# Kernel optimization log

Hardware: AMD Instinct MI355X
Metric: run time of the kernel (lower is better)

Reference implementation:

```python
import jax, jax.numpy as jnp
import numpy as np

EPS = 1e-5
HD = 16          # hidden_dim
OC = 256         # out_chs
NH = 8           # num_heads (groups of qkv conv)
DV = OC // (2 * HD)  # per-head value dim = 8


def conv_bn_silu(x, w, gamma, beta, mean, var, stride=1, pad=1, groups=1):
    # Conv2d(bias=False) + BatchNorm2d(eval) + SiLU, NCHW/OIHW
    y = jax.lax.conv_general_dilated(
        x, w, (stride, stride), [(pad, pad), (pad, pad)],
        dimension_numbers=('NCHW', 'OIHW', 'NCHW'),
        feature_group_count=groups)
    inv = gamma * jax.lax.rsqrt(var + EPS)
    y = y * inv[None, :, None, None] + (beta - mean * inv)[None, :, None, None]
    return y * jax.nn.sigmoid(y)


def _bn_params(key, c):
    k1, k2, k3, k4 = jax.random.split(key, 4)
    g = 1.0 + 0.1 * jax.random.normal(k1, (c,), jnp.float32)
    b = 0.1 * jax.random.normal(k2, (c,), jnp.float32)
    m = 0.1 * jax.random.normal(k3, (c,), jnp.float32)
    v = jax.random.uniform(k4, (c,), jnp.float32, 0.5, 1.5)
    return g, b, m, v


def setup_inputs() -> dict:
    key = jax.random.key(0)
    ks = jax.random.split(key, 8)
    B, C, H, W = 16, 256, 80, 80
    qkv_out = HD * 2 + OC // 2  # 160
    d = {}
    d['x'] = jax.random.normal(ks[0], (B, C, H, W), jnp.float32)
    # qkv_conv: grouped 3x3, groups=NH -> in per group = C//NH
    d['qkv_w'] = jax.random.normal(ks[1], (qkv_out, C // NH, 3, 3), jnp.float32) * 0.05
    d['qkv_g'], d['qkv_b'], d['qkv_m'], d['qkv_v'] = _bn_params(ks[2], qkv_out)
    # hidden_conv: dense 3x3
    d['hid_w'] = jax.random.normal(ks[3], (OC, C, 3, 3), jnp.float32) * 0.02
    d['hid_g'], d['hid_b'], d['hid_m'], d['hid_v'] = _bn_params(ks[4], OC)
    # out_conv: 1x1 on (OC//2*3) channels
    d['out_w'] = jax.random.normal(ks[5], (OC, OC // 2 * 3, 1, 1), jnp.float32) * 0.05
    d['out_g'], d['out_b'], d['out_m'], d['out_v'] = _bn_params(ks[6], OC)
    return d


def reference(x, qkv_w, qkv_g, qkv_b, qkv_m, qkv_v,
              hid_w, hid_g, hid_b, hid_m, hid_v,
              out_w, out_g, out_b, out_m, out_v):
    B, C, H, W = x.shape
    N = H * W
    qkv = conv_bn_silu(x, qkv_w, qkv_g, qkv_b, qkv_m, qkv_v, stride=1, pad=1, groups=NH)
    q = qkv[:, :HD]               # (B, HD, H, W)
    k = qkv[:, HD:2 * HD]
    v = qkv[:, 2 * HD:]           # (B, OC//2, H, W)
    # permute to (B, N, HD) / (B, N, HD, DV), channel-major reshape matches torch .view
    q = q.transpose(0, 2, 3, 1).reshape(B, N, HD)
    k = k.transpose(0, 2, 3, 1).reshape(B, N, HD)
    v = v.transpose(0, 2, 3, 1).reshape(B, N, HD, DV)
    # per-pixel tiny attention: attn[b,n,i,j] = softmax_j(q_i * k_j)
    attn = jax.nn.softmax(q[..., :, None] * k[..., None, :], axis=-1)  # (B,N,HD,HD)
    y = jnp.einsum('bnij,bnjd->bnid', attn, v)                          # (B,N,HD,DV)
    # torch: permute(0,2,3,1).view(B, OC//2, H, W)
    y = y.transpose(0, 2, 3, 1).reshape(B, OC // 2, H, W)
    h = conv_bn_silu(x, hid_w, hid_g, hid_b, hid_m, hid_v, stride=1, pad=1)
    y = jnp.concatenate([y, h], axis=1)  # (B, OC//2*3, H, W)
    return conv_bn_silu(y, out_w, out_g, out_b, out_m, out_v, stride=1, pad=0)
```

## Files before the change

### kernel.cpp

```cpp
#include <hip/hip_runtime.h>
#include <stdint.h>

typedef unsigned short u16;
typedef unsigned int u32;
typedef __attribute__((ext_vector_type(4))) float f32x4;
typedef __attribute__((ext_vector_type(8))) __bf16 bf16x8;

#define EPS_BN 1e-5f

__device__ __forceinline__ u16 f2bf(float f) {
  u32 u = __builtin_bit_cast(u32, f);
  u32 r = (u + 0x7fffu + ((u >> 16) & 1u)) >> 16;
  return (u16)r;
}

__device__ __forceinline__ float silu_f(float v) {
  return v / (1.0f + __expf(-v));
}

__device__ __forceinline__ void gll16(const void* g, void* l) {
  __builtin_amdgcn_global_load_lds(
      (__attribute__((address_space(1))) void*)(void*)g,
      (__attribute__((address_space(3))) void*)l, 16, 0, 0);
}

__global__ __launch_bounds__(256) void prep(
    const float* __restrict__ qkv_w, const float* __restrict__ qg,
    const float* __restrict__ qb, const float* __restrict__ qm,
    const float* __restrict__ qv,
    const float* __restrict__ hid_w, const float* __restrict__ hg,
    const float* __restrict__ hb, const float* __restrict__ hm,
    const float* __restrict__ hv,
    const float* __restrict__ out_w, const float* __restrict__ og,
    const float* __restrict__ ob, const float* __restrict__ om,
    const float* __restrict__ ov,
    u16* __restrict__ wtb, u16* __restrict__ w2b, u16* __restrict__ wqp,
    float* __restrict__ bnq_s, float* __restrict__ bnq_b,
    float* __restrict__ bnh_s, float* __restrict__ bnh_b,
    float* __restrict__ bn2s, float* __restrict__ bn2b,
    float* __restrict__ zpg)
{
  const int gid = blockIdx.x * 256 + threadIdx.x;
  if (gid < 256 * 2304) {
    int j = gid / 2304, k = gid - j * 2304;
    int tap = k >> 8, c = k & 255;
    wtb[gid] = f2bf(hid_w[(j * 256 + c) * 9 + tap]);
  }
  if (gid < 73728) {
    int g = gid / 9216;
    int r = gid - g * 9216;
    int j = r / 288, k = r - j * 288;
    int tap = k >> 5, cg = k & 31;
    float v = 0.f;
    if (j < 20) v = qkv_w[((g * 20 + j) * 32 + cg) * 9 + tap];
    wqp[gid] = f2bf(v);
  }
  if (gid < 98304) w2b[gid] = f2bf(out_w[gid]);
  if (gid < 160) {
    float iv = qg[gid] * rsqrtf(qv[gid] + EPS_BN);
    bnq_s[gid] = iv; bnq_b[gid] = qb[gid] - qm[gid] * iv;
  }
  if (gid < 256) {
    float iv = hg[gid] * rsqrtf(hv[gid] + EPS_BN);
    bnh_s[gid] = iv; bnh_b[gid] = hb[gid] - hm[gid] * iv;
    float iv2 = og[gid] * rsqrtf(ov[gid] + EPS_BN);
    bn2s[gid] = iv2; bn2b[gid] = ob[gid] - om[gid] * iv2;
  }
  if (gid < 64) zpg[gid] = 0.f;
}

__global__ __launch_bounds__(256) void nchw2nhwc(
    const float* __restrict__ x, u16* __restrict__ xn)
{
  __shared__ u16 T[80 * 66];
  const int t = threadIdx.x;
  const int ct = blockIdx.x;
  const int h  = blockIdx.y;
  const int b  = blockIdx.z;
  const float* src = x + ((size_t)b * 256 + ct * 64) * 6400 + h * 80;
  for (int it = 0; it < 5; ++it) {
    int idx = it * 256 + t;
    int cl = idx / 20, w4 = idx - cl * 20;
    float4 v = *(const float4*)(src + (size_t)cl * 6400 + w4 * 4);
    T[(w4 * 4 + 0) * 66 + cl] = f2bf(v.x);
    T[(w4 * 4 + 1) * 66 + cl] = f2bf(v.y);
    T[(w4 * 4 + 2) * 66 + cl] = f2bf(v.z);
    T[(w4 * 4 + 3) * 66 + cl] = f2bf(v.w);
  }
  __syncthreads();
  u16* dst = xn + ((size_t)(b * 80 + h) * 80) * 256 + ct * 64;
  for (int it = 0; it < 5; ++it) {
    int idx = it * 256 + t;
    int wl = idx >> 4;
    int cl = (idx & 15) * 4;
    ushort4 v4;
    v4.x = T[wl * 66 + cl + 0];
    v4.y = T[wl * 66 + cl + 1];
    v4.z = T[wl * 66 + cl + 2];
    v4.w = T[wl * 66 + cl + 3];
    *(ushort4*)(dst + (size_t)wl * 256 + cl) = v4;
  }
}

__global__ __launch_bounds__(256, 2) void gemm_main(
    const u16* __restrict__ xn, const u16* __restrict__ wt,
    const float* __restrict__ bns, const float* __restrict__ bnb,
    const float* __restrict__ zpg, u16* __restrict__ ycat)
{
  __shared__ __attribute__((aligned(16))) u16 Al[128 * 64];
  __shared__ __attribute__((aligned(16))) u16 Bl[128 * 64];
  const int t = threadIdx.x;
  const int wave = t >> 6, lane = t & 63;
  const int wr = wave >> 1, wc = wave & 1;
  const int orig = blockIdx.y * 2 + blockIdx.x;
  const int wg = (orig & 7) * 200 + (orig >> 3);
  const int jtile = (wg / 800) * 128;
  const int ptile = (wg % 800) * 128;

  const int srcc = (((lane & 7) ^ ((lane >> 3) & 7)) * 8);
  int pb[4], hh[4], wwv[4], bofB[4];
#pragma unroll
  for (int c = 0; c < 4; ++c) {
    int m = wave * 32 + c * 8 + (lane >> 3);
    int p = ptile + m;
    pb[c] = p;
    int hw = p % 6400;
    hh[c] = hw / 80;
    wwv[c] = hw - (hw / 80) * 80;
    bofB[c] = (jtile + m) * 2304 + srcc;
  }
  u16* AlW = Al + wave * 2048;
  u16* BlW = Bl + wave * 2048;

  f32x4 acc[4][4];
#pragma unroll
  for (int m = 0; m < 4; ++m)
#pragma unroll
    for (int n = 0; n < 4; ++n) {
      f32x4 z = {0.f, 0.f, 0.f, 0.f};
      acc[m][n] = z;
    }

  for (int ks = 0; ks < 36; ++ks) {
    const int k0 = ks * 64;
    const int tap = k0 >> 8;
    const int c0 = k0 & 255;
    const int dh = tap / 3 - 1, dw = tap - (tap / 3) * 3 - 1;
    __syncthreads();
#pragma unroll
    for (int c = 0; c < 4; ++c) {
      int h2 = hh[c] + dh, w2 = wwv[c] + dw;
      bool ok = ((unsigned)h2 < 80u) & ((unsigned)w2 < 80u);
      const u16* src = ok
          ? (xn + ((size_t)(pb[c] + dh * 80 + dw) * 256 + c0 + srcc))
          : (const u16*)zpg;
      gll16(src, AlW + c * 512);
    }
#pragma unroll
    for (int c = 0; c < 4; ++c)
      gll16(wt + (size_t)(bofB[c] + k0), BlW + c * 512);
    __syncthreads();
#pragma unroll
    for (int kk = 0; kk < 2; ++kk) {
      const int q = kk * 4 + (lane >> 4);
      const int c16 = lane & 15;
      bf16x8 av[4], bv[4];
#pragma unroll
      for (int m = 0; m < 4; ++m) {
        int r = wr * 64 + m * 16 + c16;
        av[m] = *(const bf16x8*)(Al + r * 64 + (q ^ (r & 7)) * 8);
      }
#pragma unroll
      for (int n = 0; n < 4; ++n) {
        int r = wc * 64 + n * 16 + c16;
        bv[n] = *(const bf16x8*)(Bl + r * 64 + (q ^ (r & 7)) * 8);
      }
#pragma unroll
      for (int m = 0; m < 4; ++m)
#pragma unroll
        for (int n = 0; n < 4; ++n)
          acc[m][n] = __builtin_amdgcn_mfma_f32_16x16x32_bf16(
              av[m], bv[n], acc[m][n], 0, 0, 0);
    }
  }

  const int c16 = lane & 15, rg = lane >> 4;
#pragma unroll
  for (int n = 0; n < 4; ++n) {
    int j = jtile + wc * 64 + n * 16 + c16;
    float sc = bns[j], bi = bnb[j];
#pragma unroll
    for (int m = 0; m < 4; ++m) {
      int p0 = ptile + wr * 64 + m * 16 + rg * 4;
#pragma unroll
      for (int r = 0; r < 4; ++r) {
        float v = silu_f(acc[m][n][r] * sc + bi);
        ycat[(size_t)(p0 + r) * 384 + 128 + j] = f2bf(v);
      }
    }
  }
}

__global__ __launch_bounds__(256, 2) void qkv_gemm(
    const u16* __restrict__ xn, const u16* __restrict__ wqp,
    const float* __restrict__ bnq_s, const float* __restrict__ bnq_b,
    const float* __restrict__ zpg, float* __restrict__ qkvb)
{
  __shared__ __attribute__((aligned(16))) u16 Al[2][128 * 64];
  const int t = threadIdx.x;
  const int wave = t >> 6, lane = t & 63;
  const int orig = blockIdx.x;
  const int wg = (orig & 7) * 100 + (orig >> 3);
  const int ptile = wg * 128;

  const int srcc = (((lane & 7) ^ ((lane >> 3) & 7)) * 8);
  int pb[4], hh[4], wwv[4];
#pragma unroll
  for (int c = 0; c < 4; ++c) {
    int m = wave * 32 + c * 8 + (lane >> 3);
    int p = ptile + m;
    pb[c] = p;
    int hw = p % 6400;
    hh[c] = hw / 80;
    wwv[c] = hw - (hw / 80) * 80;
  }
  u16* AlW0 = Al[0] + wave * 2048;
  u16* AlW1 = Al[1] + wave * 2048;

  const int q = lane >> 4, c16 = lane & 15;

  auto STAGE = [&](int tap, int cc, u16* dst) {
    if (tap > 8) tap = 8;
    const int dh = tap / 3 - 1, dw = tap - (tap / 3) * 3 - 1;
    const int dp = dh * 80 + dw;
    const int c0 = cc * 64;
#pragma unroll
    for (int c = 0; c < 4; ++c) {
      int h2 = hh[c] + dh, w2 = wwv[c] + dw;
      bool ok = ((unsigned)h2 < 80u) & ((unsigned)w2 < 80u);
      const u16* src = ok
          ? (xn + ((size_t)(pb[c] + dp) * 256 + c0 + srcc))
          : (const u16*)zpg;
      gll16(src, dst + c * 512);
    }
  };
  auto BQ = [&](int tap, int cc, bf16x8* bv) {
    if (tap > 8) tap = 8;
#pragma unroll
    for (int h = 0; h < 2; ++h)
#pragma unroll
      for (int nf = 0; nf < 2; ++nf) {
        int row = (2 * cc + h) * 32 + nf * 16 + c16;
        bv[h * 2 + nf] =
            *(const bf16x8*)(wqp + (size_t)row * 288 + tap * 32 + q * 8);
      }
  };

  f32x4 acc[2][16];
#pragma unroll
  for (int m = 0; m < 2; ++m)
#pragma unroll
    for (int f = 0; f < 16; ++f) {
      f32x4 z = {0.f, 0.f, 0.f, 0.f};
      acc[m][f] = z;
    }

  bf16x8 bqA[4], bqB[4];
  BQ(0, 0, bqA);
  STAGE(0, 0, AlW0);

  for (int tap = 0; tap < 9; ++tap) {
#pragma unroll
    for (int cc = 0; cc < 4; ++cc) {
      const int ntap = (cc == 3) ? tap + 1 : tap;
      const int ncc = (cc + 1) & 3;
      if ((cc & 1) == 0) { BQ(ntap, ncc, bqB); STAGE(ntap, ncc, AlW1); }
      else               { BQ(ntap, ncc, bqA); STAGE(ntap, ncc, AlW0); }
      asm volatile("s_waitcnt vmcnt(8)" ::: "memory");
      __builtin_amdgcn_sched_barrier(0);
      const u16* AW = ((cc & 1) == 0) ? AlW0 : AlW1;
      const bf16x8* bq = ((cc & 1) == 0) ? bqA : bqB;
      bf16x8 av[2][2];
#pragma unroll
      for (int m = 0; m < 2; ++m) {
        int rl = m * 16 + c16;
#pragma unroll
        for (int h = 0; h < 2; ++h) {
          int q8 = h * 4 + q;
          av[m][h] = *(const bf16x8*)(AW + rl * 64 + ((q8 ^ (rl & 7)) * 8));
        }
      }
#pragma unroll
      for (int h = 0; h < 2; ++h)
#pragma unroll
        for (int m = 0; m < 2; ++m)
#pragma unroll
          for (int nf = 0; nf < 2; ++nf)
            acc[m][(2 * cc + h) * 2 + nf] = __builtin_amdgcn_mfma_f32_16x16x32_bf16(
                av[m][h], bq[h * 2 + nf], acc[m][(2 * cc + h) * 2 + nf], 0, 0, 0);
    }
  }

#pragma unroll
  for (int f = 0; f < 16; ++f) {
    int jj = (f & 1) * 16 + c16;
    if (jj >= 20) continue;
    int oc = (f >> 1) * 20 + jj;
    float sc = bnq_s[oc], bi = bnq_b[oc];
#pragma unroll
    for (int m = 0; m < 2; ++m) {
      int p0 = ptile + wave * 32 + m * 16 + q * 4;
#pragma unroll
      for (int r = 0; r < 4; ++r)
        qkvb[(size_t)(p0 + r) * 160 + oc] = silu_f(acc[m][f][r] * sc + bi);
    }
  }
}

__global__ __launch_bounds__(256) void attn_k(
    const float* __restrict__ qkvb, u16* __restrict__ ycat)
{
  __shared__ float qs[16 * 168];
  const int t = threadIdx.x;
  const size_t p0 = (size_t)blockIdx.x * 16;
  const float* src = qkvb + p0 * 160;
  for (int idx = t; idx < 2560; idx += 256) {
    int r = idx / 160;
    qs[r * 168 + (idx - r * 160)] = src[idx];
  }
  __syncthreads();
  const int px = t >> 4, i = t & 15;
  const float* row = qs + px * 168;
  const float qi = row[i];
  float s[16];
  float mx = -3.4e38f;
#pragma unroll
  for (int j = 0; j < 16; ++j) { s[j] = qi * row[16 + j]; mx = fmaxf(mx, s[j]); }
  float sum = 0.f;
#pragma unroll
  for (int j = 0; j < 16; ++j) { s[j] = __expf(s[j] - mx); sum += s[j]; }
  const float inv = 1.0f / sum;
  float y[8];
#pragma unroll
  for (int d = 0; d < 8; ++d) y[d] = 0.f;
#pragma unroll
  for (int j = 0; j < 16; ++j) {
    const float a = s[j];
    const float* vr = row + 32 + j * 8;
#pragma unroll
    for (int d = 0; d < 8; ++d) y[d] += a * vr[d];
  }
  union { u16 u[8]; uint4 v4; } pk;
#pragma unroll
  for (int d = 0; d < 8; ++d) pk.u[d] = f2bf(y[d] * inv);
  *(uint4*)(ycat + (p0 + px) * 384 + i * 8) = pk.v4;
}

__global__ __launch_bounds__(256, 2) void gemm_out(
    const u16* __restrict__ w2, const u16* __restrict__ ycat,
    const float* __restrict__ bns, const float* __restrict__ bnb,
    float* __restrict__ out)
{
  __shared__ __attribute__((aligned(16))) u16 Al[128 * 64];
  __shared__ __attribute__((aligned(16))) u16 Bl[128 * 64];
  const int t = threadIdx.x;
  const int wave = t >> 6, lane = t & 63;
  const int wr = wave >> 1, wc = wave & 1;
  const int orig = blockIdx.y * 2 + blockIdx.x;
  const int wg = (orig & 7) * 200 + (orig >> 3);
  const int octile = (wg / 800) * 128;
  const int ptile = (wg % 800) * 128;

  const int srcc = (((lane & 7) ^ ((lane >> 3) & 7)) * 8);
  int bofA[4], bofB[4];
#pragma unroll
  for (int c = 0; c < 4; ++c) {
    int m = wave * 32 + c * 8 + (lane >> 3);
    bofA[c] = (octile + m) * 384 + srcc;
    bofB[c] = (ptile + m) * 384 + srcc;
  }
  u16* AlW = Al + wave * 2048;
  u16* BlW = Bl + wave * 2048;

  f32x4 acc[4][4];
#pragma unroll
  for (int m = 0; m < 4; ++m)
#pragma unroll
    for (int n = 0; n < 4; ++n) {
      f32x4 z = {0.f, 0.f, 0.f, 0.f};
      acc[m][n] = z;
    }

  for (int ks = 0; ks < 6; ++ks) {
    const int k0 = ks * 64;
    __syncthreads();
#pragma unroll
    for (int c = 0; c < 4; ++c) gll16(w2 + (size_t)(bofA[c] + k0), AlW + c * 512);
#pragma unroll
    for (int c = 0; c < 4; ++c) gll16(ycat + (size_t)(bofB[c] + k0), BlW + c * 512);
    __syncthreads();
#pragma unroll
    for (int kk = 0; kk < 2; ++kk) {
      const int q = kk * 4 + (lane >> 4);
      const int c16 = lane & 15;
      bf16x8 av[4], bv[4];
#pragma unroll
      for (int m = 0; m < 4; ++m) {
        int r = wr * 64 + m * 16 + c16;
        av[m] = *(const bf16x8*)(Al + r * 64 + (q ^ (r & 7)) * 8);
      }
#pragma unroll
      for (int n = 0; n < 4; ++n) {
        int r = wc * 64 + n * 16 + c16;
        bv[n] = *(const bf16x8*)(Bl + r * 64 + (q ^ (r & 7)) * 8);
      }
#pragma unroll
      for (int m = 0; m < 4; ++m)
#pragma unroll
        for (int n = 0; n < 4; ++n)
          acc[m][n] = __builtin_amdgcn_mfma_f32_16x16x32_bf16(
              av[m], bv[n], acc[m][n], 0, 0, 0);
    }
  }

  const int c16 = lane & 15, rg = lane >> 4;
  const int b = ptile / 6400;
  const int hwb = ptile - b * 6400;
#pragma unroll
  for (int m = 0; m < 4; ++m) {
    int oc0 = octile + wr * 64 + m * 16 + rg * 4;
#pragma unroll
    for (int n = 0; n < 4; ++n) {
      int hw = hwb + wc * 64 + n * 16 + c16;
#pragma unroll
      for (int r = 0; r < 4; ++r) {
        int oc = oc0 + r;
        float v = silu_f(acc[m][n][r] * bns[oc] + bnb[oc]);
        out[((size_t)b * 256 + oc) * 6400 + hw] = v;
      }
    }
  }
}

extern "C" void kernel_launch(void* const* d_in, const int* in_sizes, int n_in,
                              void* d_out, int out_size, void* d_ws, size_t ws_size,
                              hipStream_t stream) {
  (void)in_sizes; (void)n_in; (void)out_size; (void)ws_size;
  const float* x    = (const float*)d_in[0];
  const float* qkvw = (const float*)d_in[1];
  const float* qg   = (const float*)d_in[2];
  const float* qb   = (const float*)d_in[3];
  const float* qm   = (const float*)d_in[4];
  const float* qv   = (const float*)d_in[5];
  const float* hw_  = (const float*)d_in[6];
  const float* hg   = (const float*)d_in[7];
  const float* hb   = (const float*)d_in[8];
  const float* hm   = (const float*)d_in[9];
  const float* hv   = (const float*)d_in[10];
  const float* ow   = (const float*)d_in[11];
  const float* og   = (const float*)d_in[12];
  const float* ob   = (const float*)d_in[13];
  const float* om   = (const float*)d_in[14];
  const float* ov   = (const float*)d_in[15];

  char* ws = (char*)d_ws;
  float* zpg   = (float*)(ws + 0);
  float* bnq_s = (float*)(ws + 256);
  float* bnq_b = (float*)(ws + 1280);
  float* bnh_s = (float*)(ws + 2304);
  float* bnh_b = (float*)(ws + 3328);
  float* bn2s  = (float*)(ws + 4352);
  float* bn2b  = (float*)(ws + 5376);
  u16*   wtb   = (u16*)(ws + 6400);
  u16*   w2b   = (u16*)(ws + 1186048);
  u16*   wqp   = (u16*)(ws + 1382656);
  u16*   xn    = (u16*)(ws + 1536000);
  float* qkvb  = (float*)(ws + 53964800);
  u16*   ycat  = (u16*)(ws + 119500800);
  float* out   = (float*)d_out;

  prep<<<dim3(2304), dim3(256), 0, stream>>>(
      qkvw, qg, qb, qm, qv, hw_, hg, hb, hm, hv, ow, og, ob, om, ov,
      wtb, w2b, wqp, bnq_s, bnq_b, bnh_s, bnh_b, bn2s, bn2b, zpg);
  nchw2nhwc<<<dim3(4, 80, 16), dim3(256), 0, stream>>>(x, xn);
  gemm_main<<<dim3(2, 800), dim3(256), 0, stream>>>(
      xn, wtb, bnh_s, bnh_b, zpg, ycat);
  qkv_gemm<<<dim3(800), dim3(256), 0, stream>>>(
      xn, wqp, bnq_s, bnq_b, zpg, qkvb);
  attn_k<<<dim3(6400), dim3(256), 0, stream>>>(qkvb, ycat);
  gemm_out<<<dim3(2, 800), dim3(256), 0, stream>>>(
      w2b, ycat, bn2s, bn2b, out);
}
```

Measured before the change: 346.8 us.

## Double-buffer LDS tiles in hidden-conv and output GEMMs to overlap loads

```diff
diff --git a/kernel.cpp b/kernel.cpp
--- a/kernel.cpp
+++ b/kernel.cpp
@@ -107,8 +107,8 @@
     const float* __restrict__ bns, const float* __restrict__ bnb,
     const float* __restrict__ zpg, u16* __restrict__ ycat)
 {
-  __shared__ __attribute__((aligned(16))) u16 Al[128 * 64];
-  __shared__ __attribute__((aligned(16))) u16 Bl[128 * 64];
+  __shared__ __attribute__((aligned(16))) u16 Al[2][128 * 64];
+  __shared__ __attribute__((aligned(16))) u16 Bl[2][128 * 64];
   const int t = threadIdx.x;
   const int wave = t >> 6, lane = t & 63;
   const int wr = wave >> 1, wc = wave & 1;
@@ -129,24 +129,14 @@
     wwv[c] = hw - (hw / 80) * 80;
     bofB[c] = (jtile + m) * 2304 + srcc;
   }
-  u16* AlW = Al + wave * 2048;
-  u16* BlW = Bl + wave * 2048;
-
-  f32x4 acc[4][4];
-#pragma unroll
-  for (int m = 0; m < 4; ++m)
-#pragma unroll
-    for (int n = 0; n < 4; ++n) {
-      f32x4 z = {0.f, 0.f, 0.f, 0.f};
-      acc[m][n] = z;
-    }
-
-  for (int ks = 0; ks < 36; ++ks) {
+
+  auto STAGE = [&](int ks, int buf) {
     const int k0 = ks * 64;
     const int tap = k0 >> 8;
     const int c0 = k0 & 255;
     const int dh = tap / 3 - 1, dw = tap - (tap / 3) * 3 - 1;
-    __syncthreads();
+    u16* aw = Al[buf] + wave * 2048;
+    u16* bw = Bl[buf] + wave * 2048;
 #pragma unroll
     for (int c = 0; c < 4; ++c) {
       int h2 = hh[c] + dh, w2 = wwv[c] + dw;
@@ -154,26 +144,56 @@
       const u16* src = ok
           ? (xn + ((size_t)(pb[c] + dh * 80 + dw) * 256 + c0 + srcc))
           : (const u16*)zpg;
-      gll16(src, AlW + c * 512);
+      gll16(src, aw + c * 512);
     }
 #pragma unroll
     for (int c = 0; c < 4; ++c)
-      gll16(wt + (size_t)(bofB[c] + k0), BlW + c * 512);
-    __syncthreads();
+      gll16(wt + (size_t)(bofB[c] + k0), bw + c * 512);
+  };
+
+  f32x4 acc[4][4];
+#pragma unroll
+  for (int m = 0; m < 4; ++m)
+#pragma unroll
+    for (int n = 0; n < 4; ++n) {
+      f32x4 z = {0.f, 0.f, 0.f, 0.f};
+      acc[m][n] = z;
+    }
+
+  const int c16 = lane & 15, lq = lane >> 4;
+
+  STAGE(0, 0);
+  asm volatile("s_waitcnt vmcnt(0)" ::: "memory");
+  __builtin_amdgcn_sched_barrier(0);
+  __builtin_amdgcn_s_barrier();
+  __builtin_amdgcn_sched_barrier(0);
+
+  for (int ks = 0; ks < 36; ++ks) {
+    const int cur = ks & 1;
+    if (ks + 1 < 36) {
+      STAGE(ks + 1, cur ^ 1);
+      asm volatile("s_waitcnt vmcnt(8)" ::: "memory");
+    } else {
+      asm volatile("s_waitcnt vmcnt(0)" ::: "memory");
+    }
+    __builtin_amdgcn_sched_barrier(0);
+    __builtin_amdgcn_s_barrier();
+    __builtin_amdgcn_sched_barrier(0);
+    const u16* Ab = Al[cur];
+    const u16* Bb = Bl[cur];
 #pragma unroll
     for (int kk = 0; kk < 2; ++kk) {
-      const int q = kk * 4 + (lane >> 4);
-      const int c16 = lane & 15;
+      const int q = kk * 4 + lq;
       bf16x8 av[4], bv[4];
 #pragma unroll
       for (int m = 0; m < 4; ++m) {
         int r = wr * 64 + m * 16 + c16;
-        av[m] = *(const bf16x8*)(Al + r * 64 + (q ^ (r & 7)) * 8);
+        av[m] = *(const bf16x8*)(Ab + r * 64 + (q ^ (r & 7)) * 8);
       }
 #pragma unroll
       for (int n = 0; n < 4; ++n) {
         int r = wc * 64 + n * 16 + c16;
-        bv[n] = *(const bf16x8*)(Bl + r * 64 + (q ^ (r & 7)) * 8);
+        bv[n] = *(const bf16x8*)(Bb + r * 64 + (q ^ (r & 7)) * 8);
       }
 #pragma unroll
       for (int m = 0; m < 4; ++m)
@@ -182,9 +202,11 @@
           acc[m][n] = __builtin_amdgcn_mfma_f32_16x16x32_bf16(
               av[m], bv[n], acc[m][n], 0, 0, 0);
     }
-  }
-
-  const int c16 = lane & 15, rg = lane >> 4;
+    __builtin_amdgcn_s_barrier();
+    __builtin_amdgcn_sched_barrier(0);
+  }
+
+  const int rg = lq;
 #pragma unroll
   for (int n = 0; n < 4; ++n) {
     int j = jtile + wc * 64 + n * 16 + c16;
@@ -361,8 +383,8 @@
     const float* __restrict__ bns, const float* __restrict__ bnb,
     float* __restrict__ out)
 {
-  __shared__ __attribute__((aligned(16))) u16 Al[128 * 64];
-  __shared__ __attribute__((aligned(16))) u16 Bl[128 * 64];
+  __shared__ __attribute__((aligned(16))) u16 Al[2][128 * 64];
+  __shared__ __attribute__((aligned(16))) u16 Bl[2][128 * 64];
   const int t = threadIdx.x;
   const int wave = t >> 6, lane = t & 63;
   const int wr = wave >> 1, wc = wave & 1;
@@ -379,8 +401,16 @@
     bofA[c] = (octile + m) * 384 + srcc;
     bofB[c] = (ptile + m) * 384 + srcc;
   }
-  u16* AlW = Al + wave * 2048;
-  u16* BlW = Bl + wave * 2048;
+
+  auto STAGE = [&](int ks, int buf) {
+    const int k0 = ks * 64;
+    u16* aw = Al[buf] + wave * 2048;
+    u16* bw = Bl[buf] + wave * 2048;
+#pragma unroll
+    for (int c = 0; c < 4; ++c) gll16(w2 + (size_t)(bofA[c] + k0), aw + c * 512);
+#pragma unroll
+    for (int c = 0; c < 4; ++c) gll16(ycat + (size_t)(bofB[c] + k0), bw + c * 512);
+  };
 
   f32x4 acc[4][4];
 #pragma unroll
@@ -391,28 +421,40 @@
       acc[m][n] = z;
     }
 
+  const int c16 = lane & 15, lq = lane >> 4;
+
+  STAGE(0, 0);
+  asm volatile("s_waitcnt vmcnt(0)" ::: "memory");
+  __builtin_amdgcn_sched_barrier(0);
+  __builtin_amdgcn_s_barrier();
+  __builtin_amdgcn_sched_barrier(0);
+
   for (int ks = 0; ks < 6; ++ks) {
-    const int k0 = ks * 64;
-    __syncthreads();
-#pragma unroll
-    for (int c = 0; c < 4; ++c) gll16(w2 + (size_t)(bofA[c] + k0), AlW + c * 512);
-#pragma unroll
-    for (int c = 0; c < 4; ++c) gll16(ycat + (size_t)(bofB[c] + k0), BlW + c * 512);
-    __syncthreads();
+    const int cur = ks & 1;
+    if (ks + 1 < 6) {
+      STAGE(ks + 1, cur ^ 1);
+      asm volatile("s_waitcnt vmcnt(8)" ::: "memory");
+    } else {
+      asm volatile("s_waitcnt vmcnt(0)" ::: "memory");
+    }
+    __builtin_amdgcn_sched_barrier(0);
+    __builtin_amdgcn_s_barrier();
+    __builtin_amdgcn_sched_barrier(0);
+    const u16* Ab = Al[cur];
+    const u16* Bb = Bl[cur];
 #pragma unroll
     for (int kk = 0; kk < 2; ++kk) {
-      const int q = kk * 4 + (lane >> 4);
-      const int c16 = lane & 15;
+      const int q = kk * 4 + lq;
       bf16x8 av[4], bv[4];
 #pragma unroll
       for (int m = 0; m < 4; ++m) {
         int r = wr * 64 + m * 16 + c16;
-        av[m] = *(const bf16x8*)(Al + r * 64 + (q ^ (r & 7)) * 8);
+        av[m] = *(const bf16x8*)(Ab + r * 64 + (q ^ (r & 7)) * 8);
       }
 #pragma unroll
       for (int n = 0; n < 4; ++n) {
         int r = wc * 64 + n * 16 + c16;
-        bv[n] = *(const bf16x8*)(Bl + r * 64 + (q ^ (r & 7)) * 8);
+        bv[n] = *(const bf16x8*)(Bb + r * 64 + (q ^ (r & 7)) * 8);
       }
 #pragma unroll
       for (int m = 0; m < 4; ++m)
@@ -421,9 +463,11 @@
           acc[m][n] = __builtin_amdgcn_mfma_f32_16x16x32_bf16(
               av[m], bv[n], acc[m][n], 0, 0, 0);
     }
-  }
-
-  const int c16 = lane & 15, rg = lane >> 4;
+    __builtin_amdgcn_s_barrier();
+    __builtin_amdgcn_sched_barrier(0);
+  }
+
+  const int rg = lq;
   const int b = ptile / 6400;
   const int hwb = ptile - b * 6400;
 #pragma unroll
```

After: 376.9 us. 8.7% more time.

## Fuse per-pixel attention into qkv GEMM epilogue via shared memory

Applied to the files above, without the earlier changes.

```diff
diff --git a/kernel.cpp b/kernel.cpp
--- a/kernel.cpp
+++ b/kernel.cpp
@@ -201,12 +201,16 @@
   }
 }
 
-__global__ __launch_bounds__(256, 2) void qkv_gemm(
+__global__ __launch_bounds__(256, 2) void qkv_attn(
     const u16* __restrict__ xn, const u16* __restrict__ wqp,
     const float* __restrict__ bnq_s, const float* __restrict__ bnq_b,
-    const float* __restrict__ zpg, float* __restrict__ qkvb)
+    const float* __restrict__ zpg, u16* __restrict__ ycat)
 {
-  __shared__ __attribute__((aligned(16))) u16 Al[2][128 * 64];
+  __shared__ __attribute__((aligned(16))) char LB[81920];
+  u16* Al0 = (u16*)LB;
+  u16* Al1 = (u16*)(LB + 16384);
+  float* qs = (float*)LB;
+
   const int t = threadIdx.x;
   const int wave = t >> 6, lane = t & 63;
   const int orig = blockIdx.x;
@@ -224,8 +228,8 @@
     hh[c] = hw / 80;
     wwv[c] = hw - (hw / 80) * 80;
   }
-  u16* AlW0 = Al[0] + wave * 2048;
-  u16* AlW1 = Al[1] + wave * 2048;
+  u16* AlW0 = Al0 + wave * 2048;
+  u16* AlW1 = Al1 + wave * 2048;
 
   const int q = lane >> 4, c16 = lane & 15;
 
@@ -301,6 +305,10 @@
     }
   }
 
+  asm volatile("s_waitcnt vmcnt(0)" ::: "memory");
+  __builtin_amdgcn_sched_barrier(0);
+  __syncthreads();
+
 #pragma unroll
   for (int f = 0; f < 16; ++f) {
     int jj = (f & 1) * 16 + c16;
@@ -309,51 +317,42 @@
     float sc = bnq_s[oc], bi = bnq_b[oc];
 #pragma unroll
     for (int m = 0; m < 2; ++m) {
-      int p0 = ptile + wave * 32 + m * 16 + q * 4;
+      int pl0 = wave * 32 + m * 16 + q * 4;
 #pragma unroll
       for (int r = 0; r < 4; ++r)
-        qkvb[(size_t)(p0 + r) * 160 + oc] = silu_f(acc[m][f][r] * sc + bi);
-    }
-  }
-}
-
-__global__ __launch_bounds__(256) void attn_k(
-    const float* __restrict__ qkvb, u16* __restrict__ ycat)
-{
-  __shared__ float qs[16 * 168];
-  const int t = threadIdx.x;
-  const size_t p0 = (size_t)blockIdx.x * 16;
-  const float* src = qkvb + p0 * 160;
-  for (int idx = t; idx < 2560; idx += 256) {
-    int r = idx / 160;
-    qs[r * 168 + (idx - r * 160)] = src[idx];
+        qs[(pl0 + r) * 160 + oc] = silu_f(acc[m][f][r] * sc + bi);
+    }
   }
   __syncthreads();
-  const int px = t >> 4, i = t & 15;
-  const float* row = qs + px * 168;
-  const float qi = row[i];
-  float s[16];
-  float mx = -3.4e38f;
-#pragma unroll
-  for (int j = 0; j < 16; ++j) { s[j] = qi * row[16 + j]; mx = fmaxf(mx, s[j]); }
-  float sum = 0.f;
-#pragma unroll
-  for (int j = 0; j < 16; ++j) { s[j] = __expf(s[j] - mx); sum += s[j]; }
-  const float inv = 1.0f / sum;
-  float y[8];
-#pragma unroll
-  for (int d = 0; d < 8; ++d) y[d] = 0.f;
-#pragma unroll
-  for (int j = 0; j < 16; ++j) {
-    const float a = s[j];
-    const float* vr = row + 32 + j * 8;
-#pragma unroll
-    for (int d = 0; d < 8; ++d) y[d] += a * vr[d];
-  }
-  union { u16 u[8]; uint4 v4; } pk;
-#pragma unroll
-  for (int d = 0; d < 8; ++d) pk.u[d] = f2bf(y[d] * inv);
-  *(uint4*)(ycat + (p0 + px) * 384 + i * 8) = pk.v4;
+
+  for (int it = 0; it < 8; ++it) {
+    int idx = it * 256 + t;
+    int px = idx >> 4, i = idx & 15;
+    const float* row = qs + px * 160;
+    const float qi = row[i];
+    float s[16];
+    float mx = -3.4e38f;
+#pragma unroll
+    for (int j = 0; j < 16; ++j) { s[j] = qi * row[16 + j]; mx = fmaxf(mx, s[j]); }
+    float sum = 0.f;
+#pragma unroll
+    for (int j = 0; j < 16; ++j) { s[j] = __expf(s[j] - mx); sum += s[j]; }
+    const float inv = 1.0f / sum;
+    float y[8];
+#pragma unroll
+    for (int d = 0; d < 8; ++d) y[d] = 0.f;
+#pragma unroll
+    for (int j = 0; j < 16; ++j) {
+      const float a = s[j];
+      const float* vr = row + 32 + j * 8;
+#pragma unroll
+      for (int d = 0; d < 8; ++d) y[d] += a * vr[d];
+    }
+    union { u16 u[8]; uint4 v4; } pk;
+#pragma unroll
+    for (int d = 0; d < 8; ++d) pk.u[d] = f2bf(y[d] * inv);
+    *(uint4*)(ycat + (size_t)(ptile + px) * 384 + i * 8) = pk.v4;
+  }
 }
 
 __global__ __launch_bounds__(256, 2) void gemm_out(
@@ -475,7 +474,6 @@
   u16*   w2b   = (u16*)(ws + 1186048);
   u16*   wqp   = (u16*)(ws + 1382656);
   u16*   xn    = (u16*)(ws + 1536000);
-  float* qkvb  = (float*)(ws + 53964800);
   u16*   ycat  = (u16*)(ws + 119500800);
   float* out   = (float*)d_out;
 
@@ -485,9 +483,8 @@
   nchw2nhwc<<<dim3(4, 80, 16), dim3(256), 0, stream>>>(x, xn);
   gemm_main<<<dim3(2, 800), dim3(256), 0, stream>>>(
       xn, wtb, bnh_s, bnh_b, zpg, ycat);
-  qkv_gemm<<<dim3(800), dim3(256), 0, stream>>>(
-      xn, wqp, bnq_s, bnq_b, zpg, qkvb);
-  attn_k<<<dim3(6400), dim3(256), 0, stream>>>(qkvb, ycat);
+  qkv_attn<<<dim3(800), dim3(256), 0, stream>>>(
+      xn, wqp, bnq_s, bnq_b, zpg, ycat);
   gemm_out<<<dim3(2, 800), dim3(256), 0, stream>>>(
       w2b, ycat, bn2s, bn2b, out);
 }
```

Result: faster. 332.9 us (median of 2 runs) (-4.0%).
